# Optimization experiments

Hardware: AMD Instinct MI355X
Metric: run time of the kernel (lower is better)

Reference implementation:

```python
import jax, jax.numpy as jnp
import numpy as np


def _pairwise_dist(x, y):
    # x: [B, N, D], y: [B, M, D] -> Euclidean distances [B, N, M]
    # numerical safety before sqrt.
    x2 = jnp.sum(x * x, axis=-1)            # [B, N]
    y2 = jnp.sum(y * y, axis=-1)            # [B, M]
    xy = jnp.einsum('bnd,bmd->bnm', x, y)   # [B, N, M]
    d2 = x2[:, :, None] + y2[:, None, :] - 2.0 * xy
    return jnp.sqrt(jnp.maximum(d2, 0.0))


def setup_inputs() -> dict:
    key = jax.random.key(0)
    k1, k2 = jax.random.split(key)
    B, N, M, D = 4, 8192, 8192, 3
    true_pos = jax.random.normal(k1, (B, N, D), dtype=jnp.float32)
    pred_pos = jax.random.normal(k2, (B, M, D), dtype=jnp.float32)
    return {"true_pos": true_pos, "pred_pos": pred_pos}


def reference(true_pos, pred_pos):
    dists = _pairwise_dist(true_pos.astype(jnp.float32),
                           pred_pos.astype(jnp.float32))  # [B, N, M]
    mins = jnp.min(dists, axis=2)        # [B, N] nearest pred for each true
    mins_seeds = jnp.min(dists, axis=1)  # [B, M] nearest true for each pred
    loss = jnp.mean(mins)
    loss_seeds = jnp.mean(mins_seeds)
    return (loss + loss_seeds, mins_seeds)
```

## Files before the change

### kernel.cpp

```cpp
#include <hip/hip_runtime.h>

typedef __attribute__((ext_vector_type(4)))  short bf16x4;
typedef __attribute__((ext_vector_type(16))) float f32x16;

#define TPB    256
#define NPTS   8192
#define NB     4
#define TOTPTS (NB * NPTS)
#define XWAVE  64
#define XBLK   (4 * XWAVE)
#define YTILE  1024
#define NTILES (YTILE / 32)
#define GXB    (NPTS / XBLK)
#define GYB    (NPTS / YTILE)
#define NSLICE (2 * NB)
#define WS2_FLOATS ((size_t)GYB * NSLICE * NPTS)
#define NPARTIAL ((2 * TOTPTS) / 64)


__device__ __forceinline__ short bfr(float f) {
    unsigned u = __float_as_uint(f);
    return (short)((u + 0x7FFFu + ((u >> 16) & 1u)) >> 16);
}
__device__ __forceinline__ float bf2f(short s) {
    return __uint_as_float(((unsigned)(unsigned short)s) << 16);
}
__device__ __forceinline__ float min3f(float a, float b, float c) {
    float d;
    asm("v_min3_f32 %0, %1, %2, %3" : "=v"(d) : "v"(a), "v"(b), "v"(c));
    return d;
}
__device__ __forceinline__ void tree16(const f32x16& d, float& rm) {
    float u0 = min3f(d[0],  d[1],  d[2]);
    float u1 = min3f(d[3],  d[4],  d[5]);
    float u2 = min3f(d[6],  d[7],  d[8]);
    float u3 = min3f(d[9],  d[10], d[11]);
    float u4 = min3f(d[12], d[13], d[14]);
    float v0 = min3f(u0, u1, d[15]);
    float v1 = min3f(u2, u3, u4);
    asm("v_min3_f32 %0, %0, %1, %2" : "+v"(rm) : "v"(v0), "v"(v1));
}

__global__ void __launch_bounds__(TPB, 1) nnmin_mfma(
        const float* __restrict__ T, const float* __restrict__ P,
        float* __restrict__ ws2)
{
    __shared__ bf16x4 sA[NTILES * 64];

    const int z   = blockIdx.z;
    const int dir = z >> 2;
    const int b   = z & 3;
    const float* Xb = (dir ? P : T) + (size_t)b * NPTS * 3;
    const float* Yb = (dir ? T : P) + (size_t)b * NPTS * 3;
    const int t     = threadIdx.x;
    const int l     = t & 63;
    const int w     = t >> 6;
    const int ybase = blockIdx.y * YTILE;
    const int xw    = blockIdx.x * XBLK + w * XWAVE;

    for (int p = t; p < YTILE; p += TPB) {
        const float* yp = Yb + (size_t)(ybase + p) * 3;
        float y0 = yp[0], y1 = yp[1], y2 = yp[2];
        short yh0 = bfr(y0); short yl0 = bfr(y0 - bf2f(yh0));
        short yh1 = bfr(y1); short yl1 = bfr(y1 - bf2f(yh1));
        short yh2 = bfr(y2); short yl2 = bfr(y2 - bf2f(yh2));
        float hy  = 0.5f * (y0 * y0 + y1 * y1 + y2 * y2);
        short hyh = bfr(hy); short hyl = bfr(hy - bf2f(hyh));
        int tile = p >> 5, m = p & 31;
        bf16x4 e0 = {yh0, yl0, yh1, yl1};
        bf16x4 e1 = {yh2, yl2, hyh, hyl};
        sA[tile * 64 + m]      = e0;
        sA[tile * 64 + 32 + m] = e1;
    }

    const int   kh  = l >> 5;
    const short ONE = 0x3F80;
    bf16x4 B[2];
#pragma unroll
    for (int f = 0; f < 2; ++f) {
        const float* xp = Xb + (size_t)(xw + f * 32 + (l & 31)) * 3;
        short h0 = bfr(-xp[0]);
        short h1 = bfr(-xp[1]);
        short h2 = bfr(-xp[2]);
        bf16x4 e;
        if (kh == 0) e = (bf16x4){h0, h0, h1, h1};
        else         e = (bf16x4){h2, h2, ONE, ONE};
        B[f] = e;
    }
    __syncthreads();

    f32x16 zero = {0.f};
    float rm0 = 3.0e38f, rm1 = 3.0e38f;

    bf16x4 A0 = sA[l];
    bf16x4 Ab = sA[64 + l];
    f32x16 da = __builtin_amdgcn_mfma_f32_32x32x8bf16_1k(A0, B[0], zero, 0, 0, 0);
    f32x16 db = __builtin_amdgcn_mfma_f32_32x32x8bf16_1k(A0, B[1], zero, 0, 0, 0);

#pragma unroll 1
    for (int tl = 0; tl < NTILES; tl += 2) {
        bf16x4 An2 = sA[((tl + 2) & (NTILES - 1)) * 64 + l];
        bf16x4 An3 = sA[((tl + 3) & (NTILES - 1)) * 64 + l];
        f32x16 na = __builtin_amdgcn_mfma_f32_32x32x8bf16_1k(Ab, B[0], zero, 0, 0, 0);
        f32x16 nb = __builtin_amdgcn_mfma_f32_32x32x8bf16_1k(Ab, B[1], zero, 0, 0, 0);
        tree16(da, rm0);
        tree16(db, rm1);
        da = __builtin_amdgcn_mfma_f32_32x32x8bf16_1k(An2, B[0], zero, 0, 0, 0);
        db = __builtin_amdgcn_mfma_f32_32x32x8bf16_1k(An2, B[1], zero, 0, 0, 0);
        tree16(na, rm0);
        tree16(nb, rm1);
        Ab = An3;
    }

    float* o = ws2 + ((size_t)blockIdx.y * NSLICE + z) * NPTS;
    {
        float v = fminf(rm0, __shfl_xor(rm0, 32, 64));
        if (l < 32) o[xw + l] = v;
    }
    {
        float v = fminf(rm1, __shfl_xor(rm1, 32, 64));
        if (l < 32) o[xw + 32 + l] = v;
    }
}

__global__ void __launch_bounds__(TPB) finalize_kernel(
        const float* __restrict__ ws2,
        const float* __restrict__ T, const float* __restrict__ P,
        float* __restrict__ out, float* __restrict__ partials)
{
    int i   = blockIdx.x * TPB + threadIdx.x;
    int dir = (i >= TOTPTS) ? 1 : 0;
    int idx = i - dir * TOTPTS;
    int b   = idx >> 13;
    int x   = idx & (NPTS - 1);

    const float* p0 = ws2 + (size_t)(dir * 4 + b) * NPTS + x;
    float m = 3.0e38f;
#pragma unroll
    for (int c = 0; c < GYB; ++c)
        m = fminf(m, p0[(size_t)c * NSLICE * NPTS]);

    const float* xp = (dir ? P : T) + ((size_t)b * NPTS + x) * 3;
    float a0 = bf2f(bfr(xp[0]));
    float a1 = bf2f(bfr(xp[1]));
    float a2 = bf2f(bfr(xp[2]));
    float hx = 0.5f * (a0 * a0 + a1 * a1 + a2 * a2);
    float d  = sqrtf(fmaxf(2.0f * (hx + m), 0.0f));
    if (dir) out[1 + idx] = d;

#pragma unroll
    for (int off = 32; off > 0; off >>= 1)
        d += __shfl_down(d, off, 64);
    if ((threadIdx.x & 63) == 0) partials[i >> 6] = d;
}

__global__ void scalar_kernel(const float* __restrict__ partials,
                              float* __restrict__ out) {
    int t = threadIdx.x;
    float s = 0.0f;
#pragma unroll
    for (int k = 0; k < NPARTIAL / 64; ++k)
        s += partials[t + 64 * k];
#pragma unroll
    for (int off = 32; off > 0; off >>= 1)
        s += __shfl_down(s, off, 64);
    if (t == 0) out[0] = s * (1.0f / (float)TOTPTS);
}

extern "C" void kernel_launch(void* const* d_in, const int* in_sizes, int n_in,
                              void* d_out, int out_size, void* d_ws, size_t ws_size,
                              hipStream_t stream) {
    const float* truep = (const float*)d_in[0];
    const float* predp = (const float*)d_in[1];
    float* out = (float*)d_out;

    float* ws2      = (float*)d_ws;
    float* partials = ws2 + WS2_FLOATS;

    dim3 grid(GXB, GYB, 2 * NB);
    nnmin_mfma<<<grid, TPB, 0, stream>>>(truep, predp, ws2);

    finalize_kernel<<<(2 * TOTPTS) / TPB, TPB, 0, stream>>>(
        ws2, truep, predp, out, partials);
    scalar_kernel<<<1, 64, 0, stream>>>(partials, out);
}
```

Baseline: 81.87 us.

## Precompute Y bf16 fragments in a prep kernel and use single-wave blocks reading global

The per-block LDS staging of split-bf16 Y fragments is moved into a separate prep kernel that writes the fragments to workspace once per slice. The main kernel becomes single-wave blocks that read the A fragments straight from global/L2 with a two-deep register prefetch, and the explicit two-tile software pipelining is replaced by a simpler one-tile loop. This removes redundant conversion work and the block barrier, and raises block count for scheduling flexibility. In exchange it adds a kernel launch, makes operand loads go through global memory latency, and the simplified loop may expose MFMA-to-min dependency stalls.

```diff
diff --git a/kernel.cpp b/kernel.cpp
--- a/kernel.cpp
+++ b/kernel.cpp
@@ -7,15 +7,15 @@
 #define NPTS   8192
 #define NB     4
 #define TOTPTS (NB * NPTS)
-#define XWAVE  64
-#define XBLK   (4 * XWAVE)
 #define YTILE  1024
 #define NTILES (YTILE / 32)
-#define GXB    (NPTS / XBLK)
 #define GYB    (NPTS / YTILE)
 #define NSLICE (2 * NB)
+#define XW1    64
+#define GX1    (NPTS / XW1)
 #define WS2_FLOATS ((size_t)GYB * NSLICE * NPTS)
 #define NPARTIAL ((2 * TOTPTS) / 64)
+#define FRAG_OFF_FLOATS ((size_t)(4 << 20) / 4)
 
 
 __device__ __forceinline__ short bfr(float f) {
@@ -41,37 +41,41 @@
     asm("v_min3_f32 %0, %0, %1, %2" : "+v"(rm) : "v"(v0), "v"(v1));
 }
 
-__global__ void __launch_bounds__(TPB, 1) nnmin_mfma(
+__global__ void __launch_bounds__(TPB, 1) prep_frags(
         const float* __restrict__ T, const float* __restrict__ P,
-        float* __restrict__ ws2)
+        bf16x4* __restrict__ frag)
 {
-    __shared__ bf16x4 sA[NTILES * 64];
+    const int s   = blockIdx.y;
+    const int dir = s >> 2;
+    const int b   = s & 3;
+    const float* Yb = (dir ? T : P) + (size_t)b * NPTS * 3;
+    const int j = blockIdx.x * TPB + threadIdx.x;
 
+    const float* yp = Yb + (size_t)j * 3;
+    float y0 = yp[0], y1 = yp[1], y2 = yp[2];
+    short yh0 = bfr(y0); short yl0 = bfr(y0 - bf2f(yh0));
+    short yh1 = bfr(y1); short yl1 = bfr(y1 - bf2f(yh1));
+    short yh2 = bfr(y2); short yl2 = bfr(y2 - bf2f(yh2));
+    float hy  = 0.5f * (y0 * y0 + y1 * y1 + y2 * y2);
+    short hyh = bfr(hy); short hyl = bfr(hy - bf2f(hyh));
+    bf16x4 e0 = {yh0, yl0, yh1, yl1};
+    bf16x4 e1 = {yh2, yl2, hyh, hyl};
+    size_t base = ((size_t)s * NPTS + j) * 2;
+    frag[base]     = e0;
+    frag[base + 1] = e1;
+}
+
+__global__ void __launch_bounds__(64, 1) nnmin_mfma1w(
+        const float* __restrict__ T, const float* __restrict__ P,
+        const bf16x4* __restrict__ frag, float* __restrict__ ws2)
+{
     const int z   = blockIdx.z;
     const int dir = z >> 2;
     const int b   = z & 3;
     const float* Xb = (dir ? P : T) + (size_t)b * NPTS * 3;
-    const float* Yb = (dir ? T : P) + (size_t)b * NPTS * 3;
-    const int t     = threadIdx.x;
-    const int l     = t & 63;
-    const int w     = t >> 6;
+    const int l     = threadIdx.x;
     const int ybase = blockIdx.y * YTILE;
-    const int xw    = blockIdx.x * XBLK + w * XWAVE;
-
-    for (int p = t; p < YTILE; p += TPB) {
-        const float* yp = Yb + (size_t)(ybase + p) * 3;
-        float y0 = yp[0], y1 = yp[1], y2 = yp[2];
-        short yh0 = bfr(y0); short yl0 = bfr(y0 - bf2f(yh0));
-        short yh1 = bfr(y1); short yl1 = bfr(y1 - bf2f(yh1));
-        short yh2 = bfr(y2); short yl2 = bfr(y2 - bf2f(yh2));
-        float hy  = 0.5f * (y0 * y0 + y1 * y1 + y2 * y2);
-        short hyh = bfr(hy); short hyl = bfr(hy - bf2f(hyh));
-        int tile = p >> 5, m = p & 31;
-        bf16x4 e0 = {yh0, yl0, yh1, yl1};
-        bf16x4 e1 = {yh2, yl2, hyh, hyl};
-        sA[tile * 64 + m]      = e0;
-        sA[tile * 64 + 32 + m] = e1;
-    }
+    const int xw    = blockIdx.x * XW1;
 
     const int   kh  = l >> 5;
     const short ONE = 0x3F80;
@@ -87,29 +91,24 @@
         else         e = (bf16x4){h2, h2, ONE, ONE};
         B[f] = e;
     }
-    __syncthreads();
+
+    const bf16x4* fa = frag + ((size_t)z * NPTS + ybase) * 2;
+    const int i0 = (l & 31) * 2 + kh;
 
     f32x16 zero = {0.f};
     float rm0 = 3.0e38f, rm1 = 3.0e38f;
 
-    bf16x4 A0 = sA[l];
-    bf16x4 Ab = sA[64 + l];
-    f32x16 da = __builtin_amdgcn_mfma_f32_32x32x8bf16_1k(A0, B[0], zero, 0, 0, 0);
-    f32x16 db = __builtin_amdgcn_mfma_f32_32x32x8bf16_1k(A0, B[1], zero, 0, 0, 0);
-
+    bf16x4 A0 = fa[i0];
+    bf16x4 A1 = fa[64 + i0];
 #pragma unroll 1
-    for (int tl = 0; tl < NTILES; tl += 2) {
-        bf16x4 An2 = sA[((tl + 2) & (NTILES - 1)) * 64 + l];
-        bf16x4 An3 = sA[((tl + 3) & (NTILES - 1)) * 64 + l];
-        f32x16 na = __builtin_amdgcn_mfma_f32_32x32x8bf16_1k(Ab, B[0], zero, 0, 0, 0);
-        f32x16 nb = __builtin_amdgcn_mfma_f32_32x32x8bf16_1k(Ab, B[1], zero, 0, 0, 0);
+    for (int tl = 0; tl < NTILES; ++tl) {
+        bf16x4 An = fa[((tl + 2) & (NTILES - 1)) * 64 + i0];
+        f32x16 da = __builtin_amdgcn_mfma_f32_32x32x8bf16_1k(A0, B[0], zero, 0, 0, 0);
+        f32x16 db = __builtin_amdgcn_mfma_f32_32x32x8bf16_1k(A0, B[1], zero, 0, 0, 0);
         tree16(da, rm0);
         tree16(db, rm1);
-        da = __builtin_amdgcn_mfma_f32_32x32x8bf16_1k(An2, B[0], zero, 0, 0, 0);
-        db = __builtin_amdgcn_mfma_f32_32x32x8bf16_1k(An2, B[1], zero, 0, 0, 0);
-        tree16(na, rm0);
-        tree16(nb, rm1);
-        Ab = An3;
+        A0 = A1;
+        A1 = An;
     }
 
     float* o = ws2 + ((size_t)blockIdx.y * NSLICE + z) * NPTS;
@@ -176,9 +175,12 @@
 
     float* ws2      = (float*)d_ws;
     float* partials = ws2 + WS2_FLOATS;
+    bf16x4* frag    = (bf16x4*)((float*)d_ws + FRAG_OFF_FLOATS);
 
-    dim3 grid(GXB, GYB, 2 * NB);
-    nnmin_mfma<<<grid, TPB, 0, stream>>>(truep, predp, ws2);
+    prep_frags<<<dim3(NPTS / TPB, NSLICE), TPB, 0, stream>>>(truep, predp, frag);
+
+    dim3 grid(GX1, GYB, 2 * NB);
+    nnmin_mfma1w<<<grid, 64, 0, stream>>>(truep, predp, frag, ws2);
 
     finalize_kernel<<<(2 * TOTPTS) / TPB, TPB, 0, stream>>>(
         ws2, truep, predp, out, partials);
```

Result: slower. 87.90 us (+7.4%).
